# Kernel tuning notes

Measured on AMD Instinct MI355X. Metric: run time of the kernel, lower is better.

Reference implementation:

```python
import jax, jax.numpy as jnp
import numpy as np

N_NODES = 60000
N_EDGES = 240000
F_IN = 768
F_OUT = 128
HEADS = 6
LRELU_SLOPE = 0.2


def _gat_layer(x, edge_index, W, a_src, a_tgt, skip_W, bias, concat, activate):
    # x: (N, F_in); W/skip_W: (F_in, H*F); a_src/a_tgt: (H, F)
    N = x.shape[0]
    H, F = a_src.shape
    proj = (x @ W).reshape(N, H, F)                      # (N,H,F)
    s_src = jnp.einsum('nhf,hf->nh', proj, a_src)        # (N,H)
    s_tgt = jnp.einsum('nhf,hf->nh', proj, a_tgt)        # (N,H)
    src, tgt = edge_index[0], edge_index[1]
    e = jax.nn.leaky_relu(s_src[src] + s_tgt[tgt], LRELU_SLOPE)   # (E,H)
    # neighborhood-wise (per target node) stable softmax
    e_max = jax.ops.segment_max(e, tgt, num_segments=N)
    e = jnp.exp(e - e_max[tgt])
    denom = jax.ops.segment_sum(e, tgt, num_segments=N)
    alpha = e / (denom[tgt] + 1e-16)                     # (E,H)
    msg = proj[src] * alpha[:, :, None]                  # (E,H,F)
    out = jax.ops.segment_sum(msg, tgt, num_segments=N)  # (N,H,F)
    # skip connection (F != F_in so skip projection is used)
    out = out + (x @ skip_W).reshape(N, H, F)
    out = out.reshape(N, H * F) if concat else out.mean(axis=1)
    out = out + bias
    return jax.nn.elu(out) if activate else out


def setup_inputs() -> dict:
    key = jax.random.key(0)
    ks = jax.random.split(key, 20)
    d = {}
    d['x'] = jax.random.normal(ks[0], (N_NODES, F_IN), dtype=jnp.float32)
    d['edge_index'] = jax.random.randint(ks[1], (2, N_EDGES), 0, N_NODES, dtype=jnp.int32)
    HF = HEADS * F_OUT  # 768
    s = 1.0 / np.sqrt(F_IN)
    for l in range(3):
        d[f'W{l}'] = jax.random.normal(ks[2 + 5 * l], (F_IN, HF), dtype=jnp.float32) * s
        d[f'a_src{l}'] = jax.random.normal(ks[3 + 5 * l], (HEADS, F_OUT), dtype=jnp.float32) * 0.1
        d[f'a_tgt{l}'] = jax.random.normal(ks[4 + 5 * l], (HEADS, F_OUT), dtype=jnp.float32) * 0.1
        d[f'skip{l}'] = jax.random.normal(ks[5 + 5 * l], (F_IN, HF), dtype=jnp.float32) * s
        d[f'b{l}'] = jnp.zeros((HF if l < 2 else F_OUT,), dtype=jnp.float32)
    return d


def reference(x, W0, a_src0, a_tgt0, skip0, b0,
              W1, a_src1, a_tgt1, skip1, b1,
              W2, a_src2, a_tgt2, skip2, b2, edge_index):
    h = _gat_layer(x, edge_index, W0, a_src0, a_tgt0, skip0, b0, concat=True, activate=True)
    h = _gat_layer(h, edge_index, W1, a_src1, a_tgt1, skip1, b1, concat=True, activate=True)
    h = _gat_layer(h, edge_index, W2, a_src2, a_tgt2, skip2, b2, concat=False, activate=False)
    return h
```

## Files before the change

### kernel.cpp

```cpp
#include <hip/hip_runtime.h>
#include <stdint.h>

#define NODES 60000
#define NPAD  60032
#define EDGES 240000
#define KDIM  768
#define HF    768
#define FOUT  128

typedef unsigned short u16;
typedef __bf16 bf16x8 __attribute__((ext_vector_type(8)));
typedef float f32x4 __attribute__((ext_vector_type(4)));

__device__ __forceinline__ float bf2f(u16 u) {
  union { uint32_t i; float f; } v; v.i = ((uint32_t)u) << 16; return v.f;
}
__device__ __forceinline__ u16 f2bf(float f) {
  union { float f; uint32_t i; } v; v.f = f;
  return (u16)((v.i + 0x7FFF + ((v.i >> 16) & 1)) >> 16);
}

__global__ __launch_bounds__(256) void convert_x_k(const float* __restrict__ x, u16* __restrict__ xb) {
  const size_t g = ((size_t)blockIdx.x * 256 + threadIdx.x) * 4;
  if (g >= (size_t)NPAD * KDIM) return;
  ushort4 o;
  if (g < (size_t)NODES * KDIM) {
    const float4 v = *(const float4*)(x + g);
    o.x = f2bf(v.x); o.y = f2bf(v.y); o.z = f2bf(v.z); o.w = f2bf(v.w);
  } else { o.x = o.y = o.z = o.w = 0; }
  *(ushort4*)(xb + g) = o;
}

template <int MODE>
__global__ __launch_bounds__(256) void prep_wcat_k(const float* __restrict__ W, const float* __restrict__ SK,
                                                   u16* __restrict__ WT) {
  __shared__ u16 tile[32][33];
  const int n0 = blockIdx.x * 32, k0 = blockIdx.y * 32;
  const int tx = threadIdx.x & 31, ty = threadIdx.x >> 5;
#pragma unroll
  for (int r = 0; r < 32; r += 8) {
    const int k = k0 + ty + r, n = n0 + tx;
    float v;
    if (n < HF) {
      v = W[(size_t)k * HF + n];
    } else if (MODE == 0) {
      v = SK[(size_t)k * HF + (n - HF)];
    } else {
      const int f = n - HF;
      v = 0.f;
#pragma unroll
      for (int h = 0; h < 6; ++h) v += SK[(size_t)k * HF + h * FOUT + f];
      v *= (1.0f / 6.0f);
    }
    tile[ty + r][tx] = f2bf(v);
  }
  __syncthreads();
#pragma unroll
  for (int r = 0; r < 32; r += 8) {
    const int n = n0 + ty + r, k = k0 + tx;
    WT[(size_t)n * KDIM + k] = tile[tx][ty + r];
  }
}

__global__ __launch_bounds__(256) void hist_k(const int* __restrict__ tgt, int* __restrict__ deg) {
  const int e = blockIdx.x * 256 + threadIdx.x;
  if (e < EDGES) atomicAdd(&deg[tgt[e]], 1);
}

__global__ __launch_bounds__(1024) void scan_k(int* __restrict__ degcur, int* __restrict__ rp) {
  __shared__ int buf[1024];
  __shared__ int carry;
  const int tid = threadIdx.x;
  if (tid == 0) carry = 0;
  __syncthreads();
  for (int base = 0; base < NODES; base += 1024) {
    const int i = base + tid;
    const int v = (i < NODES) ? degcur[i] : 0;
    buf[tid] = v; __syncthreads();
    for (int off = 1; off < 1024; off <<= 1) {
      const int t2 = (tid >= off) ? buf[tid - off] : 0;
      __syncthreads();
      buf[tid] += t2;
      __syncthreads();
    }
    const int excl = buf[tid] - v + carry;
    if (i < NODES) { rp[i] = excl; degcur[i] = excl; }
    __syncthreads();
    if (tid == 1023) carry += buf[1023];
    __syncthreads();
  }
  if (tid == 0) rp[NODES] = carry;
}

__global__ __launch_bounds__(256) void scatter_k(const int* __restrict__ srcv, const int* __restrict__ tgt,
                                                 int* __restrict__ cur, int* __restrict__ esrc) {
  const int e = blockIdx.x * 256 + threadIdx.x;
  if (e < EDGES) {
    const int t = tgt[e];
    const int pos = atomicAdd(&cur[t], 1);
    esrc[pos] = srcv[e];
  }
}

__global__ __launch_bounds__(256) void attn_k(const int* __restrict__ rp, const int* __restrict__ esrc,
                                              const float* __restrict__ ss, const float* __restrict__ stg,
                                              float* __restrict__ alp, float* __restrict__ invd) {
  const int t = blockIdx.x * 256 + threadIdx.x;
  if (t >= NODES) return;
  const int b = rp[t], e = rp[t + 1];
  float sth[6], m[6], d[6];
#pragma unroll
  for (int h = 0; h < 6; ++h) { sth[h] = stg[t * 6 + h]; m[h] = -1e30f; d[h] = 0.f; }
  for (int j = b; j < e; ++j) {
    const int s = esrc[j];
#pragma unroll
    for (int h = 0; h < 6; ++h) {
      float sc = ss[s * 6 + h] + sth[h];
      sc = sc > 0.f ? sc : 0.2f * sc;
      m[h] = fmaxf(m[h], sc);
    }
  }
  for (int j = b; j < e; ++j) {
    const int s = esrc[j];
#pragma unroll
    for (int h = 0; h < 6; ++h) {
      float sc = ss[s * 6 + h] + sth[h];
      sc = sc > 0.f ? sc : 0.2f * sc;
      const float ev = expf(sc - m[h]);
      d[h] += ev;
      alp[(size_t)j * 6 + h] = ev;
    }
  }
#pragma unroll
  for (int h = 0; h < 6; ++h) invd[t * 6 + h] = 1.f / (d[h] + 1e-16f);
}

__global__ __launch_bounds__(256, 4) void gemm_k(const u16* __restrict__ A, const u16* __restrict__ BT,
                                                 u16* __restrict__ C,
                                                 const float* __restrict__ a_src, const float* __restrict__ a_tgt,
                                                 float* __restrict__ ss, float* __restrict__ stg,
                                                 int nbx, int ncat) {
  __shared__ u16 As[2][4096];
  __shared__ u16 Bs[2][4096];
  float* sp = (float*)&As[0][0];
  const int tid = threadIdx.x;
  const int lane = tid & 63;
  const int w = tid >> 6;
  const int wm = w >> 1, wn = w & 1;
  const int r16 = lane & 15, g4 = lane >> 4;

  const int NWG = nbx * 469;
  const int q = NWG >> 3, rr = NWG & 7;
  const int orig = blockIdx.x;
  const int xcd = orig & 7, idx = orig >> 3;
  const int wg = (xcd < rr ? xcd * (q + 1) : rr * (q + 1) + (xcd - rr) * q) + idx;
  const int bx = wg % nbx, by = wg / nbx;

  const size_t rowBase = (size_t)by * 128;
  const int colBase = bx * 128;

  const int c0 = tid, c1 = tid + 256;
  const size_t aoff0 = (rowBase + (c0 >> 2)) * KDIM + (c0 & 3) * 8;
  const size_t aoff1 = (rowBase + (c1 >> 2)) * KDIM + (c1 & 3) * 8;
  const size_t boff0 = ((size_t)(colBase + (c0 >> 2))) * KDIM + (c0 & 3) * 8;
  const size_t boff1 = ((size_t)(colBase + (c1 >> 2))) * KDIM + (c1 & 3) * 8;

  auto stage = [&](int buf, int k0) {
    __builtin_amdgcn_global_load_lds((__attribute__((address_space(1))) void*)(A + aoff0 + k0),
                                     (__attribute__((address_space(3))) void*)(&As[buf][w * 512]), 16, 0, 0);
    __builtin_amdgcn_global_load_lds((__attribute__((address_space(1))) void*)(A + aoff1 + k0),
                                     (__attribute__((address_space(3))) void*)(&As[buf][2048 + w * 512]), 16, 0, 0);
    __builtin_amdgcn_global_load_lds((__attribute__((address_space(1))) void*)(BT + boff0 + k0),
                                     (__attribute__((address_space(3))) void*)(&Bs[buf][w * 512]), 16, 0, 0);
    __builtin_amdgcn_global_load_lds((__attribute__((address_space(1))) void*)(BT + boff1 + k0),
                                     (__attribute__((address_space(3))) void*)(&Bs[buf][2048 + w * 512]), 16, 0, 0);
  };

  f32x4 acc[4][4];
#pragma unroll
  for (int i = 0; i < 4; ++i)
#pragma unroll
    for (int j = 0; j < 4; ++j) acc[i][j] = f32x4{0.f, 0.f, 0.f, 0.f};

  stage(0, 0);
  __syncthreads();
  for (int ks = 0; ks < 24; ++ks) {
    const int buf = ks & 1;
    if (ks < 23) stage(buf ^ 1, (ks + 1) * 32);
    bf16x8 af[4], bv[4];
#pragma unroll
    for (int i = 0; i < 4; ++i)
      af[i] = *(const bf16x8*)(&As[buf][(wm * 64 + i * 16 + r16) * 32 + g4 * 8]);
#pragma unroll
    for (int j = 0; j < 4; ++j)
      bv[j] = *(const bf16x8*)(&Bs[buf][(wn * 64 + j * 16 + r16) * 32 + g4 * 8]);
#pragma unroll
    for (int i = 0; i < 4; ++i)
#pragma unroll
      for (int j = 0; j < 4; ++j)
        acc[i][j] = __builtin_amdgcn_mfma_f32_16x16x32_bf16(af[i], bv[j], acc[i][j], 0, 0, 0);
    __syncthreads();
  }

#pragma unroll
  for (int i = 0; i < 4; ++i) {
    const size_t row0 = rowBase + wm * 64 + i * 16 + g4 * 4;
#pragma unroll
    for (int j = 0; j < 4; ++j) {
      const int col = colBase + wn * 64 + j * 16 + r16;
#pragma unroll
      for (int r = 0; r < 4; ++r)
        C[(row0 + r) * ncat + col] = f2bf(acc[i][j][r]);
    }
  }

  if (bx < 6) {
#pragma unroll
    for (int pass = 0; pass < 2; ++pass) {
      const float* av = (pass == 0) ? a_src : a_tgt;
      float a4[4];
#pragma unroll
      for (int j = 0; j < 4; ++j) a4[j] = av[bx * FOUT + wn * 64 + j * 16 + r16];
#pragma unroll
      for (int i = 0; i < 4; ++i) {
#pragma unroll
        for (int r = 0; r < 4; ++r) {
          float p = 0.f;
#pragma unroll
          for (int j = 0; j < 4; ++j) p += acc[i][j][r] * a4[j];
#pragma unroll
          for (int off = 1; off < 16; off <<= 1) p += __shfl_xor(p, off, 64);
          if (r16 == 0) {
            const int row = wm * 64 + i * 16 + g4 * 4 + r;
            sp[pass * 256 + wn * 128 + row] = p;
          }
        }
      }
    }
    __syncthreads();
    if (tid < 128) {
      const size_t row = rowBase + tid;
      if (row < NODES) {
        ss[row * 6 + bx] = sp[tid] + sp[128 + tid];
        stg[row * 6 + bx] = sp[256 + tid] + sp[384 + tid];
      }
    }
  }
}

template <int MODE>
__global__ __launch_bounds__(256) void aggregate_k(const u16* __restrict__ Cb, const int* __restrict__ rp,
                                                   const int* __restrict__ esrc, const float* __restrict__ alp,
                                                   const float* __restrict__ invd, const float* __restrict__ bias,
                                                   u16* __restrict__ xnext, float* __restrict__ outf) {
  constexpr int ncat = (MODE == 0) ? 1536 : 896;
  const int t = blockIdx.x * 4 + (threadIdx.x >> 6);
  const int lane = threadIdx.x & 63;
  if (t >= NODES) return;
  const int l4 = lane * 4;
  const int h0 = lane >> 5;
  float macc[3][4];
#pragma unroll
  for (int k = 0; k < 3; ++k)
#pragma unroll
    for (int c = 0; c < 4; ++c) macc[k][c] = 0.f;

  const int b = rp[t], e = rp[t + 1];
  int j = b;
  for (; j + 1 < e; j += 2) {
    const int s0 = esrc[j], s1 = esrc[j + 1];
    const float2 p0 = *(const float2*)(alp + (size_t)j * 6);
    const float2 p1 = *(const float2*)(alp + (size_t)j * 6 + 2);
    const float2 p2 = *(const float2*)(alp + (size_t)j * 6 + 4);
    const float2 q0 = *(const float2*)(alp + (size_t)(j + 1) * 6);
    const float2 q1 = *(const float2*)(alp + (size_t)(j + 1) * 6 + 2);
    const float2 q2 = *(const float2*)(alp + (size_t)(j + 1) * 6 + 4);
    const float a0[6] = {p0.x, p0.y, p1.x, p1.y, p2.x, p2.y};
    const float a1[6] = {q0.x, q0.y, q1.x, q1.y, q2.x, q2.y};
    const u16* pr0 = Cb + (size_t)s0 * ncat;
    const u16* pr1 = Cb + (size_t)s1 * ncat;
#pragma unroll
    for (int k = 0; k < 3; ++k) {
      const ushort4 v0 = *(const ushort4*)(pr0 + l4 + 256 * k);
      const ushort4 v1 = *(const ushort4*)(pr1 + l4 + 256 * k);
      const float aa0 = a0[h0 + 2 * k], aa1 = a1[h0 + 2 * k];
      macc[k][0] += aa0 * bf2f(v0.x) + aa1 * bf2f(v1.x);
      macc[k][1] += aa0 * bf2f(v0.y) + aa1 * bf2f(v1.y);
      macc[k][2] += aa0 * bf2f(v0.z) + aa1 * bf2f(v1.z);
      macc[k][3] += aa0 * bf2f(v0.w) + aa1 * bf2f(v1.w);
    }
  }
  if (j < e) {
    const int s0 = esrc[j];
    const float2 p0 = *(const float2*)(alp + (size_t)j * 6);
    const float2 p1 = *(const float2*)(alp + (size_t)j * 6 + 2);
    const float2 p2 = *(const float2*)(alp + (size_t)j * 6 + 4);
    const float a0[6] = {p0.x, p0.y, p1.x, p1.y, p2.x, p2.y};
    const u16* pr0 = Cb + (size_t)s0 * ncat;
#pragma unroll
    for (int k = 0; k < 3; ++k) {
      const ushort4 v0 = *(const ushort4*)(pr0 + l4 + 256 * k);
      const float aa0 = a0[h0 + 2 * k];
      macc[k][0] += aa0 * bf2f(v0.x);
      macc[k][1] += aa0 * bf2f(v0.y);
      macc[k][2] += aa0 * bf2f(v0.z);
      macc[k][3] += aa0 * bf2f(v0.w);
    }
  }

  float inv[3];
#pragma unroll
  for (int k = 0; k < 3; ++k) inv[k] = invd[t * 6 + h0 + 2 * k];

  if (MODE == 0) {
    const u16* sk = Cb + (size_t)t * ncat + HF;
#pragma unroll
    for (int k = 0; k < 3; ++k) {
      const ushort4 s4 = *(const ushort4*)(sk + l4 + 256 * k);
      ushort4 o;
      float v0 = macc[k][0] * inv[k] + bf2f(s4.x) + bias[l4 + 256 * k];
      float v1 = macc[k][1] * inv[k] + bf2f(s4.y) + bias[l4 + 256 * k + 1];
      float v2 = macc[k][2] * inv[k] + bf2f(s4.z) + bias[l4 + 256 * k + 2];
      float v3 = macc[k][3] * inv[k] + bf2f(s4.w) + bias[l4 + 256 * k + 3];
      o.x = f2bf(v0 > 0.f ? v0 : expm1f(v0));
      o.y = f2bf(v1 > 0.f ? v1 : expm1f(v1));
      o.z = f2bf(v2 > 0.f ? v2 : expm1f(v2));
      o.w = f2bf(v3 > 0.f ? v3 : expm1f(v3));
      *(ushort4*)(xnext + (size_t)t * HF + l4 + 256 * k) = o;
    }
  } else {
    float4 o;
    float* op = &o.x;
#pragma unroll
    for (int c = 0; c < 4; ++c) {
      const float s3 = macc[0][c] * inv[0] + macc[1][c] * inv[1] + macc[2][c] * inv[2];
      const float tot = s3 + __shfl_xor(s3, 32, 64);
      op[c] = tot * (1.0f / 6.0f);
    }
    if (lane < 32) {
      const int f = lane * 4;
      const ushort4 s4 = *(const ushort4*)(Cb + (size_t)t * ncat + HF + f);
      o.x += bf2f(s4.x) + bias[f];
      o.y += bf2f(s4.y) + bias[f + 1];
      o.z += bf2f(s4.z) + bias[f + 2];
      o.w += bf2f(s4.w) + bias[f + 3];
      *(float4*)(outf + (size_t)t * FOUT + f) = o;
    }
  }
}

#define OFF_XBF 0ull
#define OFF_CB  92209152ull
#define OFF_WT  276627456ull
#define OFF_SS  279023616ull
#define OFF_ST  280463616ull
#define OFF_ALP 281903616ull
#define OFF_RP  287663616ull
#define OFF_CUR 287903744ull
#define OFF_ESR 288143872ull

extern "C" void kernel_launch(void* const* d_in, const int* in_sizes, int n_in,
                              void* d_out, int out_size, void* d_ws, size_t ws_size,
                              hipStream_t stream) {
  const float* x = (const float*)d_in[0];
  const int ei = (in_sizes[1] == 2 * EDGES) ? 1 : 16;
  const int base = (ei == 1) ? 2 : 1;
  const float *W[3], *AS[3], *AT[3], *SK[3], *B[3];
  for (int l = 0; l < 3; ++l) {
    W[l]  = (const float*)d_in[base + 5 * l + 0];
    AS[l] = (const float*)d_in[base + 5 * l + 1];
    AT[l] = (const float*)d_in[base + 5 * l + 2];
    SK[l] = (const float*)d_in[base + 5 * l + 3];
    B[l]  = (const float*)d_in[base + 5 * l + 4];
  }
  const int* edges = (const int*)d_in[ei];
  const int* srcv = edges;
  const int* tgtv = edges + EDGES;
  float* out = (float*)d_out;

  char* ws = (char*)d_ws;
  u16* xbf = (u16*)(ws + OFF_XBF);
  u16* Cb  = (u16*)(ws + OFF_CB);
  u16* WT  = (u16*)(ws + OFF_WT);
  float* invd = (float*)(ws + OFF_WT);
  float* ss  = (float*)(ws + OFF_SS);
  float* stg = (float*)(ws + OFF_ST);
  float* alp = (float*)(ws + OFF_ALP);
  int* rp  = (int*)(ws + OFF_RP);
  int* cur = (int*)(ws + OFF_CUR);
  int* esr = (int*)(ws + OFF_ESR);

  hipMemsetAsync(cur, 0, NODES * sizeof(int), stream);
  hist_k<<<(EDGES + 255) / 256, 256, 0, stream>>>(tgtv, cur);
  scan_k<<<1, 1024, 0, stream>>>(cur, rp);
  scatter_k<<<(EDGES + 255) / 256, 256, 0, stream>>>(srcv, tgtv, cur, esr);

  convert_x_k<<<45024, 256, 0, stream>>>(x, xbf);

  for (int l = 0; l < 3; ++l) {
    const int nbx = (l < 2) ? 12 : 7;
    const int ncat = nbx * 128;
    if (l < 2)
      prep_wcat_k<0><<<dim3(48, 24), 256, 0, stream>>>(W[l], SK[l], WT);
    else
      prep_wcat_k<1><<<dim3(28, 24), 256, 0, stream>>>(W[l], SK[l], WT);
    gemm_k<<<nbx * 469, 256, 0, stream>>>(xbf, WT, Cb, AS[l], AT[l], ss, stg, nbx, ncat);
    attn_k<<<(NODES + 255) / 256, 256, 0, stream>>>(rp, esr, ss, stg, alp, invd);
    if (l < 2)
      aggregate_k<0><<<15000, 256, 0, stream>>>(Cb, rp, esr, alp, invd, B[l], xbf, nullptr);
    else
      aggregate_k<1><<<15000, 256, 0, stream>>>(Cb, rp, esr, alp, invd, B[l], nullptr, out);
  }
}
```

Measured before the change: 987.1 us.

## Rewrite GEMM as 256x256 tile, 8-wave, swizzled LDS, ping-pong pipelined kernel

Enlarges the GEMM output tile from 128x128 to 256x256, using 512 threads with a 2x4 wave layout. Each wave computes 128x64 split into four quadrant phases. The K-step grows to 64 with XOR-swizzled LDS layout to avoid bank conflicts, and global->LDS loads are issued per half-tile interleaved with MFMA phases, using explicit vmcnt waits, barriers and setprio. Node padding and the last-layer concat width are raised to fit 256-wide tiles, with the attention-score epilogue remapped accordingly. This is meant to raise data reuse and MFMA utilisation, at the cost of padding work, more register pressure, and fragile hand-scheduled synchronisation.

```diff
diff --git a/kernel.cpp b/kernel.cpp
--- a/kernel.cpp
+++ b/kernel.cpp
@@ -2,11 +2,12 @@
 #include <stdint.h>
 
 #define NODES 60000
-#define NPAD  60032
+#define NPAD  60160
 #define EDGES 240000
 #define KDIM  768
 #define HF    768
 #define FOUT  128
+#define NT    12
 
 typedef unsigned short u16;
 typedef __bf16 bf16x8 __attribute__((ext_vector_type(8)));
@@ -19,6 +20,9 @@
   union { float f; uint32_t i; } v; v.f = f;
   return (u16)((v.i + 0x7FFF + ((v.i >> 16) & 1)) >> 16);
 }
+
+#define FENCE() asm volatile("" ::: "memory")
+__device__ __forceinline__ void barx() { FENCE(); __builtin_amdgcn_s_barrier(); FENCE(); }
 
 __global__ __launch_bounds__(256) void convert_x_k(const float* __restrict__ x, u16* __restrict__ xb) {
   const size_t g = ((size_t)blockIdx.x * 256 + threadIdx.x) * 4;
@@ -45,12 +49,14 @@
       v = W[(size_t)k * HF + n];
     } else if (MODE == 0) {
       v = SK[(size_t)k * HF + (n - HF)];
-    } else {
+    } else if (n < 896) {
       const int f = n - HF;
       v = 0.f;
 #pragma unroll
       for (int h = 0; h < 6; ++h) v += SK[(size_t)k * HF + h * FOUT + f];
       v *= (1.0f / 6.0f);
+    } else {
+      v = 0.f;
     }
     tile[ty + r][tx] = f2bf(v);
   }
@@ -135,94 +141,178 @@
   for (int h = 0; h < 6; ++h) invd[t * 6 + h] = 1.f / (d[h] + 1e-16f);
 }
 
-__global__ __launch_bounds__(256, 4) void gemm_k(const u16* __restrict__ A, const u16* __restrict__ BT,
+__global__ __launch_bounds__(512, 2) void gemm_k(const u16* __restrict__ A, const u16* __restrict__ BT,
                                                  u16* __restrict__ C,
                                                  const float* __restrict__ a_src, const float* __restrict__ a_tgt,
                                                  float* __restrict__ ss, float* __restrict__ stg,
                                                  int nbx, int ncat) {
-  __shared__ u16 As[2][4096];
-  __shared__ u16 Bs[2][4096];
-  float* sp = (float*)&As[0][0];
+  __shared__ u16 Al[2][2][128 * 64];
+  __shared__ u16 Bl[2][2][128 * 64];
+  float* sp = (float*)&Al[0][0][0];
+
   const int tid = threadIdx.x;
   const int lane = tid & 63;
   const int w = tid >> 6;
-  const int wm = w >> 1, wn = w & 1;
+  const int wm = w >> 2, wn = w & 3;
   const int r16 = lane & 15, g4 = lane >> 4;
 
-  const int NWG = nbx * 469;
-  const int q = NWG >> 3, rr = NWG & 7;
+  const int gd = gridDim.x;
+  const int q = gd >> 3, rr = gd & 7;
   const int orig = blockIdx.x;
   const int xcd = orig & 7, idx = orig >> 3;
   const int wg = (xcd < rr ? xcd * (q + 1) : rr * (q + 1) + (xcd - rr) * q) + idx;
   const int bx = wg % nbx, by = wg / nbx;
 
-  const size_t rowBase = (size_t)by * 128;
-  const int colBase = bx * 128;
-
-  const int c0 = tid, c1 = tid + 256;
-  const size_t aoff0 = (rowBase + (c0 >> 2)) * KDIM + (c0 & 3) * 8;
-  const size_t aoff1 = (rowBase + (c1 >> 2)) * KDIM + (c1 & 3) * 8;
-  const size_t boff0 = ((size_t)(colBase + (c0 >> 2))) * KDIM + (c0 & 3) * 8;
-  const size_t boff1 = ((size_t)(colBase + (c1 >> 2))) * KDIM + (c1 & 3) * 8;
-
-  auto stage = [&](int buf, int k0) {
-    __builtin_amdgcn_global_load_lds((__attribute__((address_space(1))) void*)(A + aoff0 + k0),
-                                     (__attribute__((address_space(3))) void*)(&As[buf][w * 512]), 16, 0, 0);
-    __builtin_amdgcn_global_load_lds((__attribute__((address_space(1))) void*)(A + aoff1 + k0),
-                                     (__attribute__((address_space(3))) void*)(&As[buf][2048 + w * 512]), 16, 0, 0);
-    __builtin_amdgcn_global_load_lds((__attribute__((address_space(1))) void*)(BT + boff0 + k0),
-                                     (__attribute__((address_space(3))) void*)(&Bs[buf][w * 512]), 16, 0, 0);
-    __builtin_amdgcn_global_load_lds((__attribute__((address_space(1))) void*)(BT + boff1 + k0),
-                                     (__attribute__((address_space(3))) void*)(&Bs[buf][2048 + w * 512]), 16, 0, 0);
+  const size_t rowBase = (size_t)by * 256;
+  const int colBase = bx * 256;
+
+  auto stage = [&](int tile, int kind) {
+    const int h = kind & 1;
+    const int bufS = tile & 1;
+    const u16* srcBase = (kind < 2) ? A : BT;
+    const size_t rcBase = (kind < 2) ? rowBase : (size_t)colBase;
+    u16* slot = (kind < 2) ? &Al[bufS][h][0] : &Bl[bufS][h][0];
+#pragma unroll
+    for (int qq = 0; qq < 2; ++qq) {
+      const int wb = (tid + qq * 512) * 16;
+      const int rho = wb >> 7;
+      const int colb = (wb & 127) ^ ((rho & 7) << 4);
+      const size_t grow = (kind < 2)
+          ? rcBase + (size_t)((rho >> 6) << 7) + h * 64 + (rho & 63)
+          : rcBase + (size_t)((rho >> 5) << 6) + h * 32 + (rho & 31);
+      const char* gp = (const char*)srcBase + grow * (KDIM * 2) + tile * 128 + colb;
+      u16* lp = slot + ((qq * 8192 + w * 1024) >> 1);
+      __builtin_amdgcn_global_load_lds((const __attribute__((address_space(1))) void*)gp,
+                                       (__attribute__((address_space(3))) void*)lp, 16, 0, 0);
+    }
   };
 
-  f32x4 acc[4][4];
-#pragma unroll
-  for (int i = 0; i < 4; ++i)
+  auto ldA = [&](int bufc, int mh, int ii, int kk) -> bf16x8 {
+    const int rho = wm * 64 + ii * 16 + r16;
+    const int byte = rho * 128 + ((kk * 64 + g4 * 16) ^ ((r16 & 7) << 4));
+    return *(const bf16x8*)((const char*)&Al[bufc][mh][0] + byte);
+  };
+  auto ldB = [&](int bufc, int nh, int jj, int kk) -> bf16x8 {
+    const int rho = wn * 32 + jj * 16 + r16;
+    const int byte = rho * 128 + ((kk * 64 + g4 * 16) ^ ((r16 & 7) << 4));
+    return *(const bf16x8*)((const char*)&Bl[bufc][nh][0] + byte);
+  };
+
+  f32x4 acc[8][4];
+#pragma unroll
+  for (int i = 0; i < 8; ++i)
 #pragma unroll
     for (int j = 0; j < 4; ++j) acc[i][j] = f32x4{0.f, 0.f, 0.f, 0.f};
 
-  stage(0, 0);
-  __syncthreads();
-  for (int ks = 0; ks < 24; ++ks) {
-    const int buf = ks & 1;
-    if (ks < 23) stage(buf ^ 1, (ks + 1) * 32);
-    bf16x8 af[4], bv[4];
-#pragma unroll
-    for (int i = 0; i < 4; ++i)
-      af[i] = *(const bf16x8*)(&As[buf][(wm * 64 + i * 16 + r16) * 32 + g4 * 8]);
-#pragma unroll
-    for (int j = 0; j < 4; ++j)
-      bv[j] = *(const bf16x8*)(&Bs[buf][(wn * 64 + j * 16 + r16) * 32 + g4 * 8]);
-#pragma unroll
-    for (int i = 0; i < 4; ++i)
-#pragma unroll
-      for (int j = 0; j < 4; ++j)
-        acc[i][j] = __builtin_amdgcn_mfma_f32_16x16x32_bf16(af[i], bv[j], acc[i][j], 0, 0, 0);
-    __syncthreads();
-  }
-
-#pragma unroll
-  for (int i = 0; i < 4; ++i) {
-    const size_t row0 = rowBase + wm * 64 + i * 16 + g4 * 4;
+  stage(0, 0); stage(0, 1); stage(0, 2); stage(0, 3);
+  stage(1, 0); stage(1, 2); stage(1, 1);
+  asm volatile("s_waitcnt vmcnt(6)" ::: "memory");
+  barx();
+
+  bf16x8 a[4][2], b0[2][2], b1[2][2];
+
+  for (int t = 0; t < NT; ++t) {
+    const int buf = t & 1;
+#pragma unroll
+    for (int ii = 0; ii < 4; ++ii)
+#pragma unroll
+      for (int kk = 0; kk < 2; ++kk) a[ii][kk] = ldA(buf, 0, ii, kk);
+#pragma unroll
+    for (int jj = 0; jj < 2; ++jj)
+#pragma unroll
+      for (int kk = 0; kk < 2; ++kk) b0[jj][kk] = ldB(buf, 0, jj, kk);
+    if (t + 1 < NT) stage(t + 1, 3);
+    barx();
+    __builtin_amdgcn_s_setprio(1);
+#pragma unroll
+    for (int ii = 0; ii < 4; ++ii)
+#pragma unroll
+      for (int jj = 0; jj < 2; ++jj) {
+        acc[ii][jj] = __builtin_amdgcn_mfma_f32_16x16x32_bf16(a[ii][0], b0[jj][0], acc[ii][jj], 0, 0, 0);
+        acc[ii][jj] = __builtin_amdgcn_mfma_f32_16x16x32_bf16(a[ii][1], b0[jj][1], acc[ii][jj], 0, 0, 0);
+      }
+    __builtin_amdgcn_s_setprio(0);
+    __builtin_amdgcn_sched_barrier(0);
+    barx();
+#pragma unroll
+    for (int jj = 0; jj < 2; ++jj)
+#pragma unroll
+      for (int kk = 0; kk < 2; ++kk) b1[jj][kk] = ldB(buf, 1, jj, kk);
+    if (t + 2 < NT) stage(t + 2, 0);
+    barx();
+    __builtin_amdgcn_s_setprio(1);
+#pragma unroll
+    for (int ii = 0; ii < 4; ++ii)
+#pragma unroll
+      for (int jj = 0; jj < 2; ++jj) {
+        acc[ii][2 + jj] = __builtin_amdgcn_mfma_f32_16x16x32_bf16(a[ii][0], b1[jj][0], acc[ii][2 + jj], 0, 0, 0);
+        acc[ii][2 + jj] = __builtin_amdgcn_mfma_f32_16x16x32_bf16(a[ii][1], b1[jj][1], acc[ii][2 + jj], 0, 0, 0);
+      }
+    __builtin_amdgcn_s_setprio(0);
+    __builtin_amdgcn_sched_barrier(0);
+    barx();
+#pragma unroll
+    for (int ii = 0; ii < 4; ++ii)
+#pragma unroll
+      for (int kk = 0; kk < 2; ++kk) a[ii][kk] = ldA(buf, 1, ii, kk);
+    if (t + 2 < NT) stage(t + 2, 2);
+    barx();
+    __builtin_amdgcn_s_setprio(1);
+#pragma unroll
+    for (int ii = 0; ii < 4; ++ii)
+#pragma unroll
+      for (int jj = 0; jj < 2; ++jj) {
+        acc[4 + ii][2 + jj] = __builtin_amdgcn_mfma_f32_16x16x32_bf16(a[ii][0], b1[jj][0], acc[4 + ii][2 + jj], 0, 0, 0);
+        acc[4 + ii][2 + jj] = __builtin_amdgcn_mfma_f32_16x16x32_bf16(a[ii][1], b1[jj][1], acc[4 + ii][2 + jj], 0, 0, 0);
+      }
+    __builtin_amdgcn_s_setprio(0);
+    __builtin_amdgcn_sched_barrier(0);
+    barx();
+    if (t + 2 < NT) {
+      stage(t + 2, 1);
+      asm volatile("s_waitcnt vmcnt(6)" ::: "memory");
+    } else {
+      asm volatile("s_waitcnt vmcnt(0)" ::: "memory");
+    }
+    barx();
+    __builtin_amdgcn_s_setprio(1);
+#pragma unroll
+    for (int ii = 0; ii < 4; ++ii)
+#pragma unroll
+      for (int jj = 0; jj < 2; ++jj) {
+        acc[4 + ii][jj] = __builtin_amdgcn_mfma_f32_16x16x32_bf16(a[ii][0], b0[jj][0], acc[4 + ii][jj], 0, 0, 0);
+        acc[4 + ii][jj] = __builtin_amdgcn_mfma_f32_16x16x32_bf16(a[ii][1], b0[jj][1], acc[4 + ii][jj], 0, 0, 0);
+      }
+    __builtin_amdgcn_s_setprio(0);
+    __builtin_amdgcn_sched_barrier(0);
+    barx();
+  }
+
+#pragma unroll
+  for (int i = 0; i < 8; ++i) {
+    const size_t row0 = rowBase + wm * 128 + (i >> 2) * 64 + (i & 3) * 16 + g4 * 4;
 #pragma unroll
     for (int j = 0; j < 4; ++j) {
-      const int col = colBase + wn * 64 + j * 16 + r16;
+      const int col = colBase + wn * 64 + (j >> 1) * 32 + (j & 1) * 16 + r16;
 #pragma unroll
       for (int r = 0; r < 4; ++r)
         C[(row0 + r) * ncat + col] = f2bf(acc[i][j][r]);
     }
   }
 
-  if (bx < 6) {
+  if (bx < 3) {
+    const int hh = 2 * bx + (wn >> 1);
 #pragma unroll
     for (int pass = 0; pass < 2; ++pass) {
       const float* av = (pass == 0) ? a_src : a_tgt;
       float a4[4];
 #pragma unroll
-      for (int j = 0; j < 4; ++j) a4[j] = av[bx * FOUT + wn * 64 + j * 16 + r16];
-#pragma unroll
-      for (int i = 0; i < 4; ++i) {
+      for (int j = 0; j < 4; ++j) {
+        const int f = (wn & 1) * 64 + (j >> 1) * 32 + (j & 1) * 16 + r16;
+        a4[j] = av[hh * FOUT + f];
+      }
+#pragma unroll
+      for (int i = 0; i < 8; ++i) {
 #pragma unroll
         for (int r = 0; r < 4; ++r) {
           float p = 0.f;
@@ -230,19 +320,22 @@
           for (int j = 0; j < 4; ++j) p += acc[i][j][r] * a4[j];
 #pragma unroll
           for (int off = 1; off < 16; off <<= 1) p += __shfl_xor(p, off, 64);
-          if (r16 == 0) {
-            const int row = wm * 64 + i * 16 + g4 * 4 + r;
-            sp[pass * 256 + wn * 128 + row] = p;
-          }
+          if (r16 == 0) sp[(pass * 8 + w) * 128 + i * 16 + g4 * 4 + r] = p;
         }
       }
     }
-    __syncthreads();
-    if (tid < 128) {
-      const size_t row = rowBase + tid;
-      if (row < NODES) {
-        ss[row * 6 + bx] = sp[tid] + sp[128 + tid];
-        stg[row * 6 + bx] = sp[256 + tid] + sp[384 + tid];
+    barx();
+    {
+      const int row = tid & 255, hsel = tid >> 8;
+      const int wmr = row >> 7, lr = row & 127;
+      const size_t grow = rowBase + row;
+      if (grow < NODES) {
+        const int wa = wmr * 4 + hsel * 2;
+        const float vS = sp[(0 * 8 + wa) * 128 + lr] + sp[(0 * 8 + wa + 1) * 128 + lr];
+        const float vT = sp[(1 * 8 + wa) * 128 + lr] + sp[(1 * 8 + wa + 1) * 128 + lr];
+        const int head = 2 * bx + hsel;
+        ss[grow * 6 + head] = vS;
+        stg[grow * 6 + head] = vT;
       }
     }
   }
@@ -253,7 +346,7 @@
                                                    const int* __restrict__ esrc, const float* __restrict__ alp,
                                                    const float* __restrict__ invd, const float* __restrict__ bias,
                                                    u16* __restrict__ xnext, float* __restrict__ outf) {
-  constexpr int ncat = (MODE == 0) ? 1536 : 896;
+  constexpr int ncat = (MODE == 0) ? 1536 : 1024;
   const int t = blockIdx.x * 4 + (threadIdx.x >> 6);
   const int lane = threadIdx.x & 63;
   if (t >= NODES) return;
@@ -350,14 +443,14 @@
 }
 
 #define OFF_XBF 0ull
-#define OFF_CB  92209152ull
-#define OFF_WT  276627456ull
-#define OFF_SS  279023616ull
-#define OFF_ST  280463616ull
-#define OFF_ALP 281903616ull
-#define OFF_RP  287663616ull
-#define OFF_CUR 287903744ull
-#define OFF_ESR 288143872ull
+#define OFF_CB  92405760ull
+#define OFF_WT  277217280ull
+#define OFF_SS  279576576ull
+#define OFF_ST  281016576ull
+#define OFF_ALP 282456576ull
+#define OFF_RP  288216576ull
+#define OFF_CUR 288456640ull
+#define OFF_ESR 288696640ull
 
 extern "C" void kernel_launch(void* const* d_in, const int* in_sizes, int n_in,
                               void* d_out, int out_size, void* d_ws, size_t ws_size,
@@ -395,16 +488,16 @@
   scan_k<<<1, 1024, 0, stream>>>(cur, rp);
   scatter_k<<<(EDGES + 255) / 256, 256, 0, stream>>>(srcv, tgtv, cur, esr);
 
-  convert_x_k<<<45024, 256, 0, stream>>>(x, xbf);
+  convert_x_k<<<45120, 256, 0, stream>>>(x, xbf);
 
   for (int l = 0; l < 3; ++l) {
-    const int nbx = (l < 2) ? 12 : 7;
-    const int ncat = nbx * 128;
+    const int nbx = (l < 2) ? 6 : 4;
+    const int ncat = nbx * 256;
     if (l < 2)
       prep_wcat_k<0><<<dim3(48, 24), 256, 0, stream>>>(W[l], SK[l], WT);
     else
-      prep_wcat_k<1><<<dim3(28, 24), 256, 0, stream>>>(W[l], SK[l], WT);
-    gemm_k<<<nbx * 469, 256, 0, stream>>>(xbf, WT, Cb, AS[l], AT[l], ss, stg, nbx, ncat);
+      prep_wcat_k<1><<<dim3(32, 24), 256, 0, stream>>>(W[l], SK[l], WT);
+    gemm_k<<<nbx * 235, 512, 0, stream>>>(xbf, WT, Cb, AS[l], AT[l], ss, stg, nbx, ncat);
     attn_k<<<(NODES + 255) / 256, 256, 0, stream>>>(rp, esr, ss, stg, alp, invd);
     if (l < 2)
       aggregate_k<0><<<15000, 256, 0, stream>>>(Cb, rp, esr, alp, invd, B[l], xbf, nullptr);
```

Result: slower. 1.069 ms (+8.3%).

## Use 16-byte gathers with half-wave per node in aggregation; serial-chunk scan

Applied to the files above, without the earlier changes.

The aggregation kernel now assigns 32 lanes per target node instead of 64, and each lane loads 8 bf16 values (16-byte vector) per head group instead of 4. This halves the grid size and widens memory transactions for the gathered neighbour rows. The single-block scan is restructured so each thread serially sums a chunk of 59 degrees before one block-wide scan, replacing 59 sequential block scans with many barriers. The cost is more registers per lane in aggregation and uncoalesced strided per-thread chunk reads in the scan.

```diff
diff --git a/kernel.cpp b/kernel.cpp
--- a/kernel.cpp
+++ b/kernel.cpp
@@ -11,6 +11,7 @@
 typedef unsigned short u16;
 typedef __bf16 bf16x8 __attribute__((ext_vector_type(8)));
 typedef float f32x4 __attribute__((ext_vector_type(4)));
+typedef unsigned short u16x8 __attribute__((ext_vector_type(8)));
 
 __device__ __forceinline__ float bf2f(u16 u) {
   union { uint32_t i; float f; } v; v.i = ((uint32_t)u) << 16; return v.f;
@@ -68,28 +69,34 @@
 }
 
 __global__ __launch_bounds__(1024) void scan_k(int* __restrict__ degcur, int* __restrict__ rp) {
-  __shared__ int buf[1024];
-  __shared__ int carry;
+  __shared__ int ps[1024];
   const int tid = threadIdx.x;
-  if (tid == 0) carry = 0;
+  const int b = tid * 59;
+  int s = 0;
+#pragma unroll 4
+  for (int i = 0; i < 59; ++i) {
+    const int idx = b + i;
+    if (idx < NODES) s += degcur[idx];
+  }
+  ps[tid] = s;
   __syncthreads();
-  for (int base = 0; base < NODES; base += 1024) {
-    const int i = base + tid;
-    const int v = (i < NODES) ? degcur[i] : 0;
-    buf[tid] = v; __syncthreads();
-    for (int off = 1; off < 1024; off <<= 1) {
-      const int t2 = (tid >= off) ? buf[tid - off] : 0;
-      __syncthreads();
-      buf[tid] += t2;
-      __syncthreads();
-    }
-    const int excl = buf[tid] - v + carry;
-    if (i < NODES) { rp[i] = excl; degcur[i] = excl; }
+  for (int off = 1; off < 1024; off <<= 1) {
+    const int v = (tid >= off) ? ps[tid - off] : 0;
     __syncthreads();
-    if (tid == 1023) carry += buf[1023];
+    ps[tid] += v;
     __syncthreads();
   }
-  if (tid == 0) rp[NODES] = carry;
+  int excl = ps[tid] - s;
+  for (int i = 0; i < 59; ++i) {
+    const int idx = b + i;
+    if (idx < NODES) {
+      const int d = degcur[idx];
+      rp[idx] = excl;
+      degcur[idx] = excl;
+      excl += d;
+    }
+  }
+  if (tid == 1023) rp[NODES] = excl;
 }
 
 __global__ __launch_bounds__(256) void scatter_k(const int* __restrict__ srcv, const int* __restrict__ tgt,
@@ -254,16 +261,16 @@
                                                    const float* __restrict__ invd, const float* __restrict__ bias,
                                                    u16* __restrict__ xnext, float* __restrict__ outf) {
   constexpr int ncat = (MODE == 0) ? 1536 : 896;
-  const int t = blockIdx.x * 4 + (threadIdx.x >> 6);
-  const int lane = threadIdx.x & 63;
+  const int t = blockIdx.x * 8 + (threadIdx.x >> 5);
+  const int lane2 = threadIdx.x & 31;
   if (t >= NODES) return;
-  const int l4 = lane * 4;
-  const int h0 = lane >> 5;
-  float macc[3][4];
+  const int cbase = lane2 * 8;
+  const int hsel = lane2 >> 4;
+  float macc[3][8];
 #pragma unroll
   for (int k = 0; k < 3; ++k)
 #pragma unroll
-    for (int c = 0; c < 4; ++c) macc[k][c] = 0.f;
+    for (int c = 0; c < 8; ++c) macc[k][c] = 0.f;
 
   const int b = rp[t], e = rp[t + 1];
   int j = b;
@@ -281,13 +288,12 @@
     const u16* pr1 = Cb + (size_t)s1 * ncat;
 #pragma unroll
     for (int k = 0; k < 3; ++k) {
-      const ushort4 v0 = *(const ushort4*)(pr0 + l4 + 256 * k);
-      const ushort4 v1 = *(const ushort4*)(pr1 + l4 + 256 * k);
-      const float aa0 = a0[h0 + 2 * k], aa1 = a1[h0 + 2 * k];
-      macc[k][0] += aa0 * bf2f(v0.x) + aa1 * bf2f(v1.x);
-      macc[k][1] += aa0 * bf2f(v0.y) + aa1 * bf2f(v1.y);
-      macc[k][2] += aa0 * bf2f(v0.z) + aa1 * bf2f(v1.z);
-      macc[k][3] += aa0 * bf2f(v0.w) + aa1 * bf2f(v1.w);
+      const u16x8 v0 = *(const u16x8*)(pr0 + cbase + 256 * k);
+      const u16x8 v1 = *(const u16x8*)(pr1 + cbase + 256 * k);
+      const float aa0 = a0[hsel + 2 * k], aa1 = a1[hsel + 2 * k];
+#pragma unroll
+      for (int c = 0; c < 8; ++c)
+        macc[k][c] += aa0 * bf2f(v0[c]) + aa1 * bf2f(v1[c]);
     }
   }
   if (j < e) {
@@ -299,52 +305,52 @@
     const u16* pr0 = Cb + (size_t)s0 * ncat;
 #pragma unroll
     for (int k = 0; k < 3; ++k) {
-      const ushort4 v0 = *(const ushort4*)(pr0 + l4 + 256 * k);
-      const float aa0 = a0[h0 + 2 * k];
-      macc[k][0] += aa0 * bf2f(v0.x);
-      macc[k][1] += aa0 * bf2f(v0.y);
-      macc[k][2] += aa0 * bf2f(v0.z);
-      macc[k][3] += aa0 * bf2f(v0.w);
+      const u16x8 v0 = *(const u16x8*)(pr0 + cbase + 256 * k);
+      const float aa0 = a0[hsel + 2 * k];
+#pragma unroll
+      for (int c = 0; c < 8; ++c)
+        macc[k][c] += aa0 * bf2f(v0[c]);
     }
   }
 
   float inv[3];
 #pragma unroll
-  for (int k = 0; k < 3; ++k) inv[k] = invd[t * 6 + h0 + 2 * k];
+  for (int k = 0; k < 3; ++k) inv[k] = invd[t * 6 + hsel + 2 * k];
 
   if (MODE == 0) {
     const u16* sk = Cb + (size_t)t * ncat + HF;
 #pragma unroll
     for (int k = 0; k < 3; ++k) {
-      const ushort4 s4 = *(const ushort4*)(sk + l4 + 256 * k);
-      ushort4 o;
-      float v0 = macc[k][0] * inv[k] + bf2f(s4.x) + bias[l4 + 256 * k];
-      float v1 = macc[k][1] * inv[k] + bf2f(s4.y) + bias[l4 + 256 * k + 1];
-      float v2 = macc[k][2] * inv[k] + bf2f(s4.z) + bias[l4 + 256 * k + 2];
-      float v3 = macc[k][3] * inv[k] + bf2f(s4.w) + bias[l4 + 256 * k + 3];
-      o.x = f2bf(v0 > 0.f ? v0 : expm1f(v0));
-      o.y = f2bf(v1 > 0.f ? v1 : expm1f(v1));
-      o.z = f2bf(v2 > 0.f ? v2 : expm1f(v2));
-      o.w = f2bf(v3 > 0.f ? v3 : expm1f(v3));
-      *(ushort4*)(xnext + (size_t)t * HF + l4 + 256 * k) = o;
+      const u16x8 s8 = *(const u16x8*)(sk + cbase + 256 * k);
+      u16x8 o;
+#pragma unroll
+      for (int c = 0; c < 8; ++c) {
+        float v = macc[k][c] * inv[k] + bf2f(s8[c]) + bias[cbase + 256 * k + c];
+        o[c] = f2bf(v > 0.f ? v : expm1f(v));
+      }
+      *(u16x8*)(xnext + (size_t)t * HF + cbase + 256 * k) = o;
     }
   } else {
-    float4 o;
-    float* op = &o.x;
-#pragma unroll
-    for (int c = 0; c < 4; ++c) {
+    float o[8];
+#pragma unroll
+    for (int c = 0; c < 8; ++c) {
       const float s3 = macc[0][c] * inv[0] + macc[1][c] * inv[1] + macc[2][c] * inv[2];
-      const float tot = s3 + __shfl_xor(s3, 32, 64);
-      op[c] = tot * (1.0f / 6.0f);
-    }
-    if (lane < 32) {
-      const int f = lane * 4;
-      const ushort4 s4 = *(const ushort4*)(Cb + (size_t)t * ncat + HF + f);
-      o.x += bf2f(s4.x) + bias[f];
-      o.y += bf2f(s4.y) + bias[f + 1];
-      o.z += bf2f(s4.z) + bias[f + 2];
-      o.w += bf2f(s4.w) + bias[f + 3];
-      *(float4*)(outf + (size_t)t * FOUT + f) = o;
+      o[c] = (s3 + __shfl_xor(s3, 16, 64)) * (1.0f / 6.0f);
+    }
+    if (hsel == 0) {
+      const int f = cbase;
+      const u16x8 s8 = *(const u16x8*)(Cb + (size_t)t * ncat + HF + f);
+      float4 o0, o1;
+      o0.x = o[0] + bf2f(s8[0]) + bias[f + 0];
+      o0.y = o[1] + bf2f(s8[1]) + bias[f + 1];
+      o0.z = o[2] + bf2f(s8[2]) + bias[f + 2];
+      o0.w = o[3] + bf2f(s8[3]) + bias[f + 3];
+      o1.x = o[4] + bf2f(s8[4]) + bias[f + 4];
+      o1.y = o[5] + bf2f(s8[5]) + bias[f + 5];
+      o1.z = o[6] + bf2f(s8[6]) + bias[f + 6];
+      o1.w = o[7] + bf2f(s8[7]) + bias[f + 7];
+      *(float4*)(outf + (size_t)t * FOUT + f) = o0;
+      *(float4*)(outf + (size_t)t * FOUT + f + 4) = o1;
     }
   }
 }
@@ -407,8 +413,8 @@
     gemm_k<<<nbx * 469, 256, 0, stream>>>(xbf, WT, Cb, AS[l], AT[l], ss, stg, nbx, ncat);
     attn_k<<<(NODES + 255) / 256, 256, 0, stream>>>(rp, esr, ss, stg, alp, invd);
     if (l < 2)
-      aggregate_k<0><<<15000, 256, 0, stream>>>(Cb, rp, esr, alp, invd, B[l], xbf, nullptr);
+      aggregate_k<0><<<7500, 256, 0, stream>>>(Cb, rp, esr, alp, invd, B[l], xbf, nullptr);
     else
-      aggregate_k<1><<<15000, 256, 0, stream>>>(Cb, rp, esr, alp, invd, B[l], nullptr, out);
-  }
-}
+      aggregate_k<1><<<7500, 256, 0, stream>>>(Cb, rp, esr, alp, invd, B[l], nullptr, out);
+  }
+}
```

Result: slower. 1.146 ms (+16.1%).
